# Performance work log

Hardware: AMD Instinct MI355X
Metric: run time of the kernel (lower is better)

Reference implementation:

```python
import jax, jax.numpy as jnp
import numpy as np

DIM = 1024
NUM_HEADS = 16
HEAD_DIM = DIM // NUM_HEADS
ROPE_THETA = 10000.0
SCALE = HEAD_DIM ** -0.5


def _apply_rope(x, cos, sin):
    # x: [B, H, S, head_dim]; cos/sin: [S, head_dim//2] (broadcast over B, H)
    x_even = x[..., 0::2]
    x_odd = x[..., 1::2]
    rot_even = x_even * cos - x_odd * sin
    rot_odd = x_even * sin + x_odd * cos
    # interleave back: stack on last axis then flatten, matching torch .stack(-1).flatten(-2)
    return jnp.stack([rot_even, rot_odd], axis=-1).reshape(x.shape)


def setup_inputs() -> dict:
    key = jax.random.key(0)
    k0, k1, k2 = jax.random.split(key, 3)
    B, S = 2, 2048
    x = jax.random.normal(k0, (B, S, DIM), dtype=jnp.float32)
    # small_init: std = sqrt(2 / (5*dim))
    qkv_w = jax.random.normal(k1, (3 * DIM, DIM), dtype=jnp.float32) * (2.0 / (5 * DIM)) ** 0.5
    qkv_b = jnp.zeros((3 * DIM,), dtype=jnp.float32)
    # wang_init: std = 2 / num_blocks / sqrt(dim) scaled
    out_w = jax.random.normal(k2, (DIM, DIM), dtype=jnp.float32) * (2.0 / DIM) ** 0.5 / 2.0
    out_b = jnp.zeros((DIM,), dtype=jnp.float32)
    return {"x": x, "qkv_w": qkv_w, "qkv_b": qkv_b, "out_w": out_w, "out_b": out_b, "window_size": 512}


def reference(x, qkv_w, qkv_b, out_w, out_b, window_size):
    B, S, D = x.shape
    qkv = x @ qkv_w.T + qkv_b                          # [B, S, 3D]
    qkv = qkv.reshape(B, S, 3, NUM_HEADS, HEAD_DIM).transpose(2, 0, 3, 1, 4)
    q, k, v = qkv[0], qkv[1], qkv[2]                   # each [B, H, S, hd]

    pos = jnp.arange(S, dtype=jnp.float32)
    inv_freq = 1.0 / (ROPE_THETA ** (jnp.arange(0, HEAD_DIM, 2, dtype=jnp.float32) / HEAD_DIM))
    freqs = pos[:, None] * inv_freq                    # [S, hd//2]
    cos, sin = jnp.cos(freqs), jnp.sin(freqs)
    q = _apply_rope(q, cos, sin)
    k = _apply_rope(k, cos, sin)

    scores = jnp.einsum('bhqd,bhkd->bhqk', q, k) * SCALE
    i = jnp.arange(S)
    mask = (i[:, None] >= i[None, :]) & ((i[:, None] - i[None, :]) < window_size)  # causal sliding window
    scores = jnp.where(mask, scores, -jnp.inf)
    attn = jax.nn.softmax(scores, axis=-1)
    out = jnp.einsum('bhqk,bhkd->bhqd', attn, v)       # [B, H, S, hd]
    out = out.transpose(0, 2, 1, 3).reshape(B, S, D)
    return out @ out_w.T + out_b
```

## Files before the change

kernel.cpp:

```cpp
#include <hip/hip_runtime.h>
#include <hip/hip_bf16.h>
#include <cstdint>
#include <cstddef>

using bf16x8 = __attribute__((ext_vector_type(8))) short;
using f32x4  = __attribute__((ext_vector_type(4))) float;

#define MFMA16(a, b, c) __builtin_amdgcn_mfma_f32_16x16x32_bf16((a), (b), (c), 0, 0, 0)

__device__ __forceinline__ unsigned short f2bf(float f) {
    unsigned int u = __float_as_uint(f);
    u += 0x7fffu + ((u >> 16) & 1u);
    return (unsigned short)(u >> 16);
}
__device__ __forceinline__ uint32_t pack2bf(float a, float b) {
    __hip_bfloat162 h = __float22bfloat162_rn(float2{a, b});
    return *(uint32_t*)&h;
}
__device__ __forceinline__ float bf2f(short x) {
    return __uint_as_float(((uint32_t)(unsigned short)x) << 16);
}

__device__ __forceinline__ void gload_lds16(const void* g, void* l) {
    __builtin_amdgcn_global_load_lds(
        (const __attribute__((address_space(1))) void*)g,
        (__attribute__((address_space(3))) void*)l, 16, 0, 0);
}

#define S_LEN 2048
#define NHEAD 16
#define HDIM  64
#define DIM   1024
#define WIN   512
#define MROWS 4096

__global__ void prep(float* __restrict__ cosT, float* __restrict__ sinT,
                     const float* __restrict__ x, unsigned short* __restrict__ xb,
                     const float* __restrict__ qw, unsigned short* __restrict__ qwb,
                     const float* __restrict__ ow, unsigned short* __restrict__ owb) {
    int t = blockIdx.x * 256 + threadIdx.x;
    if (t < 65536) {
        int s = t >> 5, f = t & 31;
        float invf = powf(10000.0f, -(float)f / 32.0f);
        float ang = (float)s * invf;
        cosT[t] = cosf(ang);
        sinT[t] = sinf(ang);
        return;
    }
    int u = t - 65536;
    const float* src;
    unsigned short* dst;
    int i;
    if (u < 1048576)        { src = x;  dst = xb;  i = u * 4; }
    else if (u < 1835008)   { src = qw; dst = qwb; i = (u - 1048576) * 4; }
    else                    { src = ow; dst = owb; i = (u - 1835008) * 4; }
    float4 v = *(const float4*)(src + i);
    ushort4 o;
    o.x = f2bf(v.x); o.y = f2bf(v.y); o.z = f2bf(v.z); o.w = f2bf(v.w);
    *(ushort4*)(dst + i) = o;
}

__global__ __launch_bounds__(256) void gemm_qkv_fused(
        const unsigned short* __restrict__ A,
        const unsigned short* __restrict__ Bw,
        const float* __restrict__ bias,
        const float* __restrict__ cosT, const float* __restrict__ sinT,
        unsigned short* __restrict__ qbuf,
        unsigned short* __restrict__ kbuf,
        unsigned short* __restrict__ vtb) {
    __shared__ __align__(16) char smem_raw[34816];
    const int tid = threadIdx.x;
    const int lane = tid & 63, w = tid >> 6;
    const int wr = w >> 1, wc = w & 1, lm = lane & 15, lg = lane >> 4;
    const int bx = blockIdx.x, by = blockIdx.y;
    const int row0 = by * 128, col0 = bx * 128;
    const int plane = bx >> 3;
    const int h0 = (bx & 7) * 2;
    const int b = by >> 4, s_base = (by & 15) * 128;

    f32x4 acc[4][4];
#pragma unroll
    for (int m = 0; m < 4; ++m)
#pragma unroll
        for (int n = 0; n < 4; ++n) acc[m][n] = (f32x4){0.f, 0.f, 0.f, 0.f};

    auto As = [&](int buf) { return (short*)(smem_raw + buf * 16384); };
    auto Bs = [&](int buf) { return (short*)(smem_raw + buf * 16384 + 8192); };

    const size_t ldb = 2048;
    auto stage = [&](int kt, int buf) {
#pragma unroll
        for (int i = 0; i < 2; ++i) {
            int c = tid + 256 * i;
            int r = c >> 2, gp = c & 3;
            int gs = gp ^ ((r >> 1) & 3);
            gload_lds16((const char*)A  + (size_t)(row0 + r) * ldb + (size_t)kt * 64 + gs * 16, As(buf) + c * 8);
            gload_lds16((const char*)Bw + (size_t)(col0 + r) * ldb + (size_t)kt * 64 + gs * 16, Bs(buf) + c * 8);
        }
    };

    stage(0, 0);
    __syncthreads();
    int cur = 0;
    const int swz = (lm >> 1) & 3;
    for (int kt = 0; kt < 32; ++kt) {
        if (kt + 1 < 32) stage(kt + 1, cur ^ 1);
        bf16x8 af[4], bfr[4];
        const short* as = As(cur);
        const short* bs = Bs(cur);
#pragma unroll
        for (int m = 0; m < 4; ++m) af[m]  = *(const bf16x8*)&as[(wr * 64 + m * 16 + lm) * 32 + ((lg ^ swz) << 3)];
#pragma unroll
        for (int n = 0; n < 4; ++n) bfr[n] = *(const bf16x8*)&bs[(wc * 64 + n * 16 + lm) * 32 + ((lg ^ swz) << 3)];
#pragma unroll
        for (int m = 0; m < 4; ++m)
#pragma unroll
            for (int n = 0; n < 4; ++n) acc[m][n] = MFMA16(af[m], bfr[n], acc[m][n]);
        __syncthreads();
        cur ^= 1;
    }

    unsigned short (*tile)[136] = (unsigned short(*)[136])smem_raw;
    const int lane8 = tid & 7, idx = tid >> 3;

    if (plane < 2) {
#pragma unroll
        for (int m = 0; m < 4; ++m)
#pragma unroll
            for (int n = 0; n < 4; ++n) {
                int colL = wc * 64 + n * 16 + lm;
                float bv = bias[col0 + colL];
#pragma unroll
                for (int r = 0; r < 4; ++r)
                    tile[wr * 64 + m * 16 + lg * 4 + r][colL] = f2bf(acc[m][n][r] + bv);
            }
    } else {
#pragma unroll
        for (int m = 0; m < 4; ++m)
#pragma unroll
            for (int n = 0; n < 4; ++n) {
                int colL = wc * 64 + n * 16 + lm;
                float bv = bias[col0 + colL];
                uint2 pk;
                pk.x = pack2bf(acc[m][n][0] + bv, acc[m][n][1] + bv);
                pk.y = pack2bf(acc[m][n][2] + bv, acc[m][n][3] + bv);
                *(uint2*)&tile[colL][wr * 64 + m * 16 + lg * 4] = pk;
            }
    }
    __syncthreads();

    if (plane < 2) {
        unsigned short* dstp = (plane == 0) ? qbuf : kbuf;
        const float qsc = (plane == 0) ? 0.125f : 1.0f;
        int d0 = lane8 * 8;
#pragma unroll
        for (int j = 0; j < 4; ++j) {
            int srow = idx + 32 * j;
            int s = s_base + srow;
            float4 c4 = *(const float4*)&cosT[s * 32 + (d0 >> 1)];
            float4 s4 = *(const float4*)&sinT[s * 32 + (d0 >> 1)];
#pragma unroll
            for (int hh = 0; hh < 2; ++hh) {
                bf16x8 v = *(const bf16x8*)&tile[srow][hh * 64 + d0];
                float e0 = bf2f(v[0]), o0 = bf2f(v[1]);
                float e1 = bf2f(v[2]), o1 = bf2f(v[3]);
                float e2 = bf2f(v[4]), o2 = bf2f(v[5]);
                float e3 = bf2f(v[6]), o3 = bf2f(v[7]);
                uint4 pk;
                pk.x = pack2bf((e0 * c4.x - o0 * s4.x) * qsc, (e0 * s4.x + o0 * c4.x) * qsc);
                pk.y = pack2bf((e1 * c4.y - o1 * s4.y) * qsc, (e1 * s4.y + o1 * c4.y) * qsc);
                pk.z = pack2bf((e2 * c4.z - o2 * s4.z) * qsc, (e2 * s4.z + o2 * c4.z) * qsc);
                pk.w = pack2bf((e3 * c4.w - o3 * s4.w) * qsc, (e3 * s4.w + o3 * c4.w) * qsc);
                int h = h0 + hh;
                *(uint4*)&dstp[(((size_t)(b * NHEAD + h)) * S_LEN + s) * 64 + d0] = pk;
            }
        }
    } else {
#pragma unroll
        for (int rr = 0; rr < 4; ++rr) {
            int hd = rr * 32 + idx;
            int hh = hd >> 6, d = hd & 63, h = h0 + hh;
#pragma unroll
            for (int j = 0; j < 2; ++j) {
                int s0 = lane8 * 8 + j * 64;
                bf16x8 v = *(const bf16x8*)&tile[hd][s0];
                *(bf16x8*)&vtb[((size_t)(b * NHEAD + h) * 64 + d) * S_LEN +
                               s_base + s0] = v;
            }
        }
    }
}

__global__ __launch_bounds__(256) void gemm_out(const unsigned short* __restrict__ A,
                                                const unsigned short* __restrict__ Bw,
                                                const float* __restrict__ bias,
                                                float* __restrict__ Cout) {
    __shared__ __align__(16) char smem_raw[32768];
    const int tid = threadIdx.x;
    const int lane = tid & 63, w = tid >> 6;
    const int wr = w >> 1, wc = w & 1, lm = lane & 15, lg = lane >> 4;
    const int row0 = blockIdx.y * 128, col0 = blockIdx.x * 128;

    f32x4 acc[4][4];
#pragma unroll
    for (int m = 0; m < 4; ++m)
#pragma unroll
        for (int n = 0; n < 4; ++n) acc[m][n] = (f32x4){0.f, 0.f, 0.f, 0.f};

    auto As = [&](int buf) { return (short*)(smem_raw + buf * 16384); };
    auto Bs = [&](int buf) { return (short*)(smem_raw + buf * 16384 + 8192); };

    const size_t ldb = 2048;
    auto stage = [&](int kt, int buf) {
#pragma unroll
        for (int i = 0; i < 2; ++i) {
            int c = tid + 256 * i;
            int r = c >> 2, gp = c & 3;
            int gs = gp ^ ((r >> 1) & 3);
            gload_lds16((const char*)A  + (size_t)(row0 + r) * ldb + (size_t)kt * 64 + gs * 16, As(buf) + c * 8);
            gload_lds16((const char*)Bw + (size_t)(col0 + r) * ldb + (size_t)kt * 64 + gs * 16, Bs(buf) + c * 8);
        }
    };

    stage(0, 0);
    __syncthreads();
    int cur = 0;
    const int swz = (lm >> 1) & 3;
    for (int kt = 0; kt < 32; ++kt) {
        if (kt + 1 < 32) stage(kt + 1, cur ^ 1);
        bf16x8 af[4], bfr[4];
        const short* as = As(cur);
        const short* bs = Bs(cur);
#pragma unroll
        for (int m = 0; m < 4; ++m) af[m]  = *(const bf16x8*)&as[(wr * 64 + m * 16 + lm) * 32 + ((lg ^ swz) << 3)];
#pragma unroll
        for (int n = 0; n < 4; ++n) bfr[n] = *(const bf16x8*)&bs[(wc * 64 + n * 16 + lm) * 32 + ((lg ^ swz) << 3)];
#pragma unroll
        for (int m = 0; m < 4; ++m)
#pragma unroll
            for (int n = 0; n < 4; ++n) acc[m][n] = MFMA16(af[m], bfr[n], acc[m][n]);
        __syncthreads();
        cur ^= 1;
    }

#pragma unroll
    for (int m = 0; m < 4; ++m) {
        int row = row0 + wr * 64 + m * 16 + lg * 4;
#pragma unroll
        for (int n = 0; n < 4; ++n) {
            int col = col0 + wc * 64 + n * 16 + lm;
            float bv = bias[col];
#pragma unroll
            for (int r = 0; r < 4; ++r)
                Cout[(size_t)(row + r) * DIM + col] = acc[m][n][r] + bv;
        }
    }
}

__global__ __launch_bounds__(256) void attn(const unsigned short* __restrict__ qb,
                                            const unsigned short* __restrict__ kb,
                                            const unsigned short* __restrict__ vt,
                                            unsigned short* __restrict__ ao) {
    const int p = blockIdx.x;
    const int L = (p & 7) * 64 + (p >> 3);
    const int qbk = L & 15, bh = L >> 4;
    const int b = bh >> 4, h = bh & 15;
    const int tid = threadIdx.x, w = tid >> 6, lane = tid & 63;
    const int lm = lane & 15, lg = lane >> 4;
    const unsigned short* Qb = qb + (size_t)bh * S_LEN * 64;
    const unsigned short* Kb = kb + (size_t)bh * S_LEN * 64;
    const unsigned short* Vt = vt + (size_t)bh * 64 * S_LEN;
    const int q0w = qbk * 128 + w * 32;

    __shared__ short Ks[2][64 * 64];
    __shared__ short Vs[2][64 * 64];
    __shared__ short Plds[4][32 * 64];
    short* Pw = Plds[w];

    bf16x8 aq[2][2];
#pragma unroll
    for (int mi = 0; mi < 2; ++mi) {
        aq[mi][0] = *(const bf16x8*)&Qb[(q0w + mi * 16 + lm) * 64 + lg * 8];
        aq[mi][1] = *(const bf16x8*)&Qb[(q0w + mi * 16 + lm) * 64 + lg * 8 + 32];
    }

    f32x4 o[2][4];
#pragma unroll
    for (int mi = 0; mi < 2; ++mi)
#pragma unroll
        for (int n = 0; n < 4; ++n) o[mi][n] = (f32x4){0.f, 0.f, 0.f, 0.f};
    float lsum0 = 0.f, lsum1 = 0.f;

    const int t0 = (qbk >= 4) ? (2 * qbk - 8) : 0;
    const int t1 = 2 * qbk + 1;

    auto stage = [&](int kt, int buf) {
#pragma unroll
        for (int i = 0; i < 2; ++i) {
            int c = tid + 256 * i;
            int r = c >> 3, g = (c & 7) ^ (r & 7);
            gload_lds16(Kb + (size_t)(kt * 64 + r) * 64 + g * 8, &Ks[buf][c * 8]);
            gload_lds16(Vt + (size_t)r * S_LEN + kt * 64 + g * 8, &Vs[buf][c * 8]);
        }
    };

    stage(t0, 0);
    __syncthreads();
    int cur = 0;
    const int sw = lm & 7;
    for (int kt = t0; kt <= t1; ++kt) {
        if (kt < t1) stage(kt + 1, cur ^ 1);
        const int kbase = kt * 64;
        f32x4 sT[2][4];
#pragma unroll
        for (int n = 0; n < 4; ++n) {
            int rl = n * 16 + lm;
            bf16x8 bk0 = *(const bf16x8*)&Ks[cur][rl * 64 + ((lg ^ sw) << 3)];
            bf16x8 bk1 = *(const bf16x8*)&Ks[cur][rl * 64 + (((lg + 4) ^ sw) << 3)];
#pragma unroll
            for (int mi = 0; mi < 2; ++mi) {
                f32x4 z = (f32x4){0.f, 0.f, 0.f, 0.f};
                z = MFMA16(bk0, aq[mi][0], z);
                sT[mi][n] = MFMA16(bk1, aq[mi][1], z);
            }
        }
#pragma unroll
        for (int mi = 0; mi < 2; ++mi) {
            const int qq = q0w + mi * 16 + lm;
#pragma unroll
            for (int n = 0; n < 4; ++n) {
                int kk0 = kbase + n * 16 + lg * 4;
#pragma unroll
                for (int r = 0; r < 4; ++r) {
                    int d = qq - (kk0 + r);
                    float pv = ((unsigned)d < (unsigned)WIN) ? __expf(sT[mi][n][r]) : 0.f;
                    sT[mi][n][r] = pv;
                    if (mi == 0) lsum0 += pv; else lsum1 += pv;
                }
                uint2 pk;
                pk.x = pack2bf(sT[mi][n][0], sT[mi][n][1]);
                pk.y = pack2bf(sT[mi][n][2], sT[mi][n][3]);
                *(uint2*)&Pw[(mi * 16 + lm) * 64 +
                             ((((2 * n + (lg >> 1)) ^ sw) << 3) + ((lg & 1) << 2))] = pk;
            }
        }
        bf16x8 ap[2][2];
#pragma unroll
        for (int mi = 0; mi < 2; ++mi) {
            ap[mi][0] = *(const bf16x8*)&Pw[(mi * 16 + lm) * 64 + ((lg ^ sw) << 3)];
            ap[mi][1] = *(const bf16x8*)&Pw[(mi * 16 + lm) * 64 + (((lg + 4) ^ sw) << 3)];
        }
#pragma unroll
        for (int n = 0; n < 4; ++n) {
            int rl = n * 16 + lm;
            bf16x8 bv0 = *(const bf16x8*)&Vs[cur][rl * 64 + ((lg ^ sw) << 3)];
            bf16x8 bv1 = *(const bf16x8*)&Vs[cur][rl * 64 + (((lg + 4) ^ sw) << 3)];
#pragma unroll
            for (int mi = 0; mi < 2; ++mi) {
                o[mi][n] = MFMA16(ap[mi][0], bv0, o[mi][n]);
                o[mi][n] = MFMA16(ap[mi][1], bv1, o[mi][n]);
            }
        }
        __syncthreads();
        cur ^= 1;
    }
    lsum0 += __shfl_xor(lsum0, 16, 64);
    lsum0 += __shfl_xor(lsum0, 32, 64);
    lsum1 += __shfl_xor(lsum1, 16, 64);
    lsum1 += __shfl_xor(lsum1, 32, 64);
    float linv0 = 1.f / lsum0, linv1 = 1.f / lsum1;
#pragma unroll
    for (int mi = 0; mi < 2; ++mi) {
        float lv = (mi == 0) ? linv0 : linv1;
#pragma unroll
        for (int r = 0; r < 4; ++r) {
            float lr = __shfl(lv, lg * 4 + r, 64);
            int row = b * S_LEN + q0w + mi * 16 + lg * 4 + r;
#pragma unroll
            for (int n = 0; n < 4; ++n) {
                int col = h * 64 + n * 16 + lm;
                ao[(size_t)row * DIM + col] = f2bf(o[mi][n][r] * lr);
            }
        }
    }
}

extern "C" void kernel_launch(void* const* d_in, const int* in_sizes, int n_in,
                              void* d_out, int out_size, void* d_ws, size_t ws_size,
                              hipStream_t stream) {
    const float* x      = (const float*)d_in[0];
    const float* qkv_w  = (const float*)d_in[1];
    const float* qkv_b  = (const float*)d_in[2];
    const float* out_w  = (const float*)d_in[3];
    const float* out_b  = (const float*)d_in[4];
    (void)in_sizes; (void)n_in; (void)out_size; (void)ws_size;

    char* ws = (char*)d_ws;
    float*          cosT = (float*)(ws + 0);
    float*          sinT = (float*)(ws + 262144);
    unsigned short* xb   = (unsigned short*)(ws + 524288);
    unsigned short* wqb  = (unsigned short*)(ws + 8912896);
    unsigned short* owb  = (unsigned short*)(ws + 15204352);
    unsigned short* qbuf = (unsigned short*)(ws + 17301504);
    unsigned short* kbuf = (unsigned short*)(ws + 25690112);
    unsigned short* vtb  = (unsigned short*)(ws + 34078720);
    unsigned short* aob  = (unsigned short*)(ws + 42467328);

    prep<<<8448, 256, 0, stream>>>(cosT, sinT, x, xb, qkv_w, wqb, out_w, owb);

    gemm_qkv_fused<<<dim3(24, 32), 256, 0, stream>>>(xb, wqb, qkv_b, cosT, sinT,
                                                     qbuf, kbuf, vtb);

    attn<<<512, 256, 0, stream>>>(qbuf, kbuf, vtb, aob);

    gemm_out<<<dim3(8, 32), 256, 0, stream>>>(aob, owb, out_b, (float*)d_out);
}
```

Before: 105.9 us.

## Switch GEMMs to single-buffered 64-wide K tiles and halve out-GEMM N tile

Both the QKV and output GEMMs drop the double-buffered 32-element K staging in favour of a single-buffered 64-element K tile, using an 8-way XOR swizzle and two MFMAs per fragment pair per iteration. This halves the number of K iterations and barriers. The output GEMM also narrows its N tile from 128 to 64 and doubles its grid to 512 blocks, aiming for better CU occupancy on a small problem. The cost is that global loads no longer overlap compute, since each iteration loads and then waits at a barrier before the MFMAs run.

Result: faster. 97.96 us (-7.5%).

```diff
diff --git a/kernel.cpp b/kernel.cpp
--- a/kernel.cpp
+++ b/kernel.cpp
@@ -84,40 +84,39 @@
 #pragma unroll
         for (int n = 0; n < 4; ++n) acc[m][n] = (f32x4){0.f, 0.f, 0.f, 0.f};
 
-    auto As = [&](int buf) { return (short*)(smem_raw + buf * 16384); };
-    auto Bs = [&](int buf) { return (short*)(smem_raw + buf * 16384 + 8192); };
-
-    const size_t ldb = 2048;
-    auto stage = [&](int kt, int buf) {
-#pragma unroll
-        for (int i = 0; i < 2; ++i) {
+    short* As = (short*)smem_raw;
+    short* Bs = (short*)(smem_raw + 16384);
+
+    for (int kt = 0; kt < 16; ++kt) {
+#pragma unroll
+        for (int i = 0; i < 4; ++i) {
             int c = tid + 256 * i;
-            int r = c >> 2, gp = c & 3;
-            int gs = gp ^ ((r >> 1) & 3);
-            gload_lds16((const char*)A  + (size_t)(row0 + r) * ldb + (size_t)kt * 64 + gs * 16, As(buf) + c * 8);
-            gload_lds16((const char*)Bw + (size_t)(col0 + r) * ldb + (size_t)kt * 64 + gs * 16, Bs(buf) + c * 8);
-        }
-    };
-
-    stage(0, 0);
-    __syncthreads();
-    int cur = 0;
-    const int swz = (lm >> 1) & 3;
-    for (int kt = 0; kt < 32; ++kt) {
-        if (kt + 1 < 32) stage(kt + 1, cur ^ 1);
-        bf16x8 af[4], bfr[4];
-        const short* as = As(cur);
-        const short* bs = Bs(cur);
-#pragma unroll
-        for (int m = 0; m < 4; ++m) af[m]  = *(const bf16x8*)&as[(wr * 64 + m * 16 + lm) * 32 + ((lg ^ swz) << 3)];
-#pragma unroll
-        for (int n = 0; n < 4; ++n) bfr[n] = *(const bf16x8*)&bs[(wc * 64 + n * 16 + lm) * 32 + ((lg ^ swz) << 3)];
+            int r = c >> 3, gs = (c & 7) ^ (r & 7);
+            gload_lds16((const char*)A  + (size_t)(row0 + r) * 2048 + (size_t)kt * 128 + gs * 16, As + c * 8);
+            gload_lds16((const char*)Bw + (size_t)(col0 + r) * 2048 + (size_t)kt * 128 + gs * 16, Bs + c * 8);
+        }
+        __syncthreads();
+        bf16x8 af0[4], af1[4], bf0[4], bf1[4];
+#pragma unroll
+        for (int m = 0; m < 4; ++m) {
+            int rl = wr * 64 + m * 16 + lm, rb = rl & 7;
+            af0[m] = *(const bf16x8*)&As[rl * 64 + ((lg ^ rb) << 3)];
+            af1[m] = *(const bf16x8*)&As[rl * 64 + (((lg + 4) ^ rb) << 3)];
+        }
+#pragma unroll
+        for (int n = 0; n < 4; ++n) {
+            int rl = wc * 64 + n * 16 + lm, rb = rl & 7;
+            bf0[n] = *(const bf16x8*)&Bs[rl * 64 + ((lg ^ rb) << 3)];
+            bf1[n] = *(const bf16x8*)&Bs[rl * 64 + (((lg + 4) ^ rb) << 3)];
+        }
 #pragma unroll
         for (int m = 0; m < 4; ++m)
 #pragma unroll
-            for (int n = 0; n < 4; ++n) acc[m][n] = MFMA16(af[m], bfr[n], acc[m][n]);
+            for (int n = 0; n < 4; ++n) {
+                acc[m][n] = MFMA16(af0[m], bf0[n], acc[m][n]);
+                acc[m][n] = MFMA16(af1[m], bf1[n], acc[m][n]);
+            }
         __syncthreads();
-        cur ^= 1;
     }
 
     unsigned short (*tile)[136] = (unsigned short(*)[136])smem_raw;
@@ -195,60 +194,64 @@
                                                 const unsigned short* __restrict__ Bw,
                                                 const float* __restrict__ bias,
                                                 float* __restrict__ Cout) {
-    __shared__ __align__(16) char smem_raw[32768];
+    __shared__ __align__(16) char smem_raw[24576];
     const int tid = threadIdx.x;
     const int lane = tid & 63, w = tid >> 6;
     const int wr = w >> 1, wc = w & 1, lm = lane & 15, lg = lane >> 4;
-    const int row0 = blockIdx.y * 128, col0 = blockIdx.x * 128;
-
-    f32x4 acc[4][4];
+    const int row0 = blockIdx.y * 128, col0 = blockIdx.x * 64;
+
+    f32x4 acc[4][2];
 #pragma unroll
     for (int m = 0; m < 4; ++m)
 #pragma unroll
-        for (int n = 0; n < 4; ++n) acc[m][n] = (f32x4){0.f, 0.f, 0.f, 0.f};
-
-    auto As = [&](int buf) { return (short*)(smem_raw + buf * 16384); };
-    auto Bs = [&](int buf) { return (short*)(smem_raw + buf * 16384 + 8192); };
-
-    const size_t ldb = 2048;
-    auto stage = [&](int kt, int buf) {
+        for (int n = 0; n < 2; ++n) acc[m][n] = (f32x4){0.f, 0.f, 0.f, 0.f};
+
+    short* As = (short*)smem_raw;
+    short* Bs = (short*)(smem_raw + 16384);
+
+    for (int kt = 0; kt < 16; ++kt) {
+#pragma unroll
+        for (int i = 0; i < 4; ++i) {
+            int c = tid + 256 * i;
+            int r = c >> 3, gs = (c & 7) ^ (r & 7);
+            gload_lds16((const char*)A + (size_t)(row0 + r) * 2048 + (size_t)kt * 128 + gs * 16, As + c * 8);
+        }
 #pragma unroll
         for (int i = 0; i < 2; ++i) {
             int c = tid + 256 * i;
-            int r = c >> 2, gp = c & 3;
-            int gs = gp ^ ((r >> 1) & 3);
-            gload_lds16((const char*)A  + (size_t)(row0 + r) * ldb + (size_t)kt * 64 + gs * 16, As(buf) + c * 8);
-            gload_lds16((const char*)Bw + (size_t)(col0 + r) * ldb + (size_t)kt * 64 + gs * 16, Bs(buf) + c * 8);
-        }
-    };
-
-    stage(0, 0);
-    __syncthreads();
-    int cur = 0;
-    const int swz = (lm >> 1) & 3;
-    for (int kt = 0; kt < 32; ++kt) {
-        if (kt + 1 < 32) stage(kt + 1, cur ^ 1);
-        bf16x8 af[4], bfr[4];
-        const short* as = As(cur);
-        const short* bs = Bs(cur);
-#pragma unroll
-        for (int m = 0; m < 4; ++m) af[m]  = *(const bf16x8*)&as[(wr * 64 + m * 16 + lm) * 32 + ((lg ^ swz) << 3)];
-#pragma unroll
-        for (int n = 0; n < 4; ++n) bfr[n] = *(const bf16x8*)&bs[(wc * 64 + n * 16 + lm) * 32 + ((lg ^ swz) << 3)];
+            int r = c >> 3, gs = (c & 7) ^ (r & 7);
+            gload_lds16((const char*)Bw + (size_t)(col0 + r) * 2048 + (size_t)kt * 128 + gs * 16, Bs + c * 8);
+        }
+        __syncthreads();
+        bf16x8 af0[4], af1[4], bf0[2], bf1[2];
+#pragma unroll
+        for (int m = 0; m < 4; ++m) {
+            int rl = wr * 64 + m * 16 + lm, rb = rl & 7;
+            af0[m] = *(const bf16x8*)&As[rl * 64 + ((lg ^ rb) << 3)];
+            af1[m] = *(const bf16x8*)&As[rl * 64 + (((lg + 4) ^ rb) << 3)];
+        }
+#pragma unroll
+        for (int n = 0; n < 2; ++n) {
+            int rl = wc * 32 + n * 16 + lm, rb = rl & 7;
+            bf0[n] = *(const bf16x8*)&Bs[rl * 64 + ((lg ^ rb) << 3)];
+            bf1[n] = *(const bf16x8*)&Bs[rl * 64 + (((lg + 4) ^ rb) << 3)];
+        }
 #pragma unroll
         for (int m = 0; m < 4; ++m)
 #pragma unroll
-            for (int n = 0; n < 4; ++n) acc[m][n] = MFMA16(af[m], bfr[n], acc[m][n]);
+            for (int n = 0; n < 2; ++n) {
+                acc[m][n] = MFMA16(af0[m], bf0[n], acc[m][n]);
+                acc[m][n] = MFMA16(af1[m], bf1[n], acc[m][n]);
+            }
         __syncthreads();
-        cur ^= 1;
     }
 
 #pragma unroll
     for (int m = 0; m < 4; ++m) {
         int row = row0 + wr * 64 + m * 16 + lg * 4;
 #pragma unroll
-        for (int n = 0; n < 4; ++n) {
-            int col = col0 + wc * 64 + n * 16 + lm;
+        for (int n = 0; n < 2; ++n) {
+            int col = col0 + wc * 32 + n * 16 + lm;
             float bv = bias[col];
 #pragma unroll
             for (int r = 0; r < 4; ++r)
@@ -413,5 +416,5 @@
 
     attn<<<512, 256, 0, stream>>>(qbuf, kbuf, vtb, aob);
 
-    gemm_out<<<dim3(8, 32), 256, 0, stream>>>(aob, owb, out_b, (float*)d_out);
-}
+    gemm_out<<<dim3(16, 32), 256, 0, stream>>>(aob, owb, out_b, (float*)d_out);
+}
```
